# Performance work log

Measured on AMD Instinct MI355X. Metric: run time of the kernel, lower is better.

Reference implementation:

```python
import jax, jax.numpy as jnp
import numpy as np

N = 4096
IN_F = 256
OUT_F = 128
H = 2
ALPHA = 0.2  # leaky relu slope
NEG_INF = -9e15  # matches -9000000000000000.0 in the torch code


def setup_inputs() -> dict:
    key = jax.random.key(0)
    k_x, k_adj, k_w, k_a = jax.random.split(key, 4)
    x = jax.random.normal(k_x, (N, IN_F), dtype=jnp.float32)
    adj = (jax.random.uniform(k_adj, (N, N)) < 0.005).astype(jnp.float32)
    # xavier_uniform with gain=1.414 as in the torch module
    gain = 1.414
    bound_w = gain * np.sqrt(6.0 / (IN_F + OUT_F))
    W = jax.random.uniform(k_w, (H, IN_F, OUT_F), minval=-bound_w, maxval=bound_w, dtype=jnp.float32)
    bound_a = gain * np.sqrt(6.0 / (2 * OUT_F + 1))
    a = jax.random.uniform(k_a, (H, 2 * OUT_F, 1), minval=-bound_a, maxval=bound_a, dtype=jnp.float32)
    return {"x": x, "adj": adj, "W": W, "a": a}


def reference(x, adj, W, a):
    # Dense multi-head GAT layer (eval mode: dropout is identity).
    n = x.shape[0]
    h, _, f_out = W.shape
    adj = adj + jnp.eye(n, dtype=adj.dtype)  # add self loops
    xt = jnp.einsum('nf,hfo->hno', x, W)  # [H, N, F_out]
    # The repeat_interleave/repeat + concat + matmul(a) in the original is
    # exactly the additive decomposition: score[h,i,j] = xt[h,i]@a1[h] + xt[h,j]@a2[h]
    a1 = a[:, :f_out, 0]   # [H, F_out] (applied to target/query node i)
    a2 = a[:, f_out:, 0]   # [H, F_out] (applied to source node j)
    e1 = jnp.einsum('hno,ho->hn', xt, a1)  # [H, N]
    e2 = jnp.einsum('hno,ho->hn', xt, a2)  # [H, N]
    scores = jax.nn.leaky_relu(e1[:, :, None] + e2[:, None, :], negative_slope=ALPHA)  # [H,N,N]
    scores = jnp.where(adj > 0, scores, jnp.asarray(NEG_INF, scores.dtype))
    attn = jax.nn.softmax(scores, axis=-1)
    h_prime = jnp.einsum('hij,hjo->hio', attn, xt)  # [H, N, F_out]
    # concat=True branch: torch .view(N, H*F_out) on contiguous [H,N,F] -> same as reshape
    return jax.nn.elu(h_prime.reshape(n, h * f_out))
```

## Files before the change

kernel.cpp:

```cpp
#include <hip/hip_runtime.h>
#include <math.h>

#define IN_F 256
#define OUT_F 128
#define NHEAD 2
#define ALPHA 0.2f
#define NN 4096
#define NCAP 128

typedef __attribute__((ext_vector_type(8))) short short8;
typedef __attribute__((ext_vector_type(4))) float f32x4;
typedef const __attribute__((address_space(1))) void* gas_ptr;
typedef __attribute__((address_space(3))) void* las_ptr;

__device__ __forceinline__ void async_copy16(const void* g, void* l) {
  __builtin_amdgcn_global_load_lds((gas_ptr)g, (las_ptr)l, 16, 0, 0);
}

__device__ __forceinline__ ushort f2bf(float f) {
  unsigned u = __float_as_uint(f);
  u += 0x7fffu + ((u >> 16) & 1u);
  return (ushort)(u >> 16);
}

__device__ __forceinline__ float lrelu(float t) { return t > 0.f ? t : ALPHA * t; }

__global__ __launch_bounds__(256) void prep_w(
    const float* __restrict__ W, ushort* __restrict__ Wt) {
  int p = blockIdx.x * 256 + threadIdx.x;
  int h = p >> 13;
  int rem = p & 8191;
  int c = rem >> 7;
  int o = rem & 127;
  const float* wsrc = W + h * (IN_F * OUT_F) + (4 * c) * OUT_F + o;
  ushort4 ov;
  ov.x = f2bf(wsrc[0 * OUT_F]);
  ov.y = f2bf(wsrc[1 * OUT_F]);
  ov.z = f2bf(wsrc[2 * OUT_F]);
  ov.w = f2bf(wsrc[3 * OUT_F]);
  *(ushort4*)(Wt + ((size_t)h * OUT_F + o) * IN_F + 4 * c) = ov;
}

__global__ __launch_bounds__(256) void gemm_mfma(
    const float* __restrict__ x, const ushort* __restrict__ Wt,
    const float* __restrict__ a,
    float* __restrict__ xt, float* __restrict__ e1, float* __restrict__ e2) {
  __shared__ ushort sA[32 * 64];
  __shared__ ushort sB[128 * 64];
  __shared__ float sa[2 * OUT_F];
  __shared__ float se1[32], se2[32];

  const int h = blockIdx.y;
  const int rowBase = blockIdx.x * 32;
  const int tid = threadIdx.x;
  const int wave = tid >> 6, lane = tid & 63;
  const int wr = wave & 1, wc = wave >> 1;
  const int q = lane >> 4, l16 = lane & 15;
  const int ar = tid >> 3;
  const int ak = (tid & 7) * 8;

  const float* xrow = x + (size_t)(rowBase + ar) * IN_F + ak;
  float4 ax[8];
#pragma unroll
  for (int c = 0; c < 4; ++c) {
    ax[2 * c]     = *(const float4*)(xrow + 64 * c);
    ax[2 * c + 1] = *(const float4*)(xrow + 64 * c + 4);
  }

  sa[tid] = a[h * (2 * OUT_F) + tid];

  f32x4 acc[4];
#pragma unroll
  for (int i = 0; i < 4; ++i) acc[i] = (f32x4)(0.0f);

  const char* wbase = (const char*)(Wt + (size_t)h * (OUT_F * IN_F));

#pragma unroll
  for (int c = 0; c < 4; ++c) {
    const int k0 = c * 64;
#pragma unroll
    for (int it = 0; it < 4; ++it) {
      int g = it * 256 + tid;
      int r = g >> 3, c8 = g & 7;
      async_copy16(wbase + r * 512 + k0 * 2 + c8 * 16,
                   (char*)sB + (size_t)(it * 256 + wave * 64) * 16);
    }
    {
      float4 va = ax[2 * c], vb = ax[2 * c + 1];
      union { short8 s8; ushort u[8]; } pk;
      pk.u[0] = f2bf(va.x); pk.u[1] = f2bf(va.y);
      pk.u[2] = f2bf(va.z); pk.u[3] = f2bf(va.w);
      pk.u[4] = f2bf(vb.x); pk.u[5] = f2bf(vb.y);
      pk.u[6] = f2bf(vb.z); pk.u[7] = f2bf(vb.w);
      *(short8*)(sA + ar * 64 + ak) = pk.s8;
    }
    __syncthreads();

#pragma unroll
    for (int ks = 0; ks < 64; ks += 32) {
      short8 af = *(const short8*)(sA + (wr * 16 + l16) * 64 + ks + q * 8);
#pragma unroll
      for (int ct = 0; ct < 4; ++ct) {
        int col = wc * 64 + ct * 16 + l16;
        short8 bf = *(const short8*)(sB + col * 64 + ks + q * 8);
        acc[ct] = __builtin_amdgcn_mfma_f32_16x16x32_bf16(af, bf, acc[ct], 0, 0, 0);
      }
    }
    __syncthreads();
  }

#pragma unroll
  for (int ct = 0; ct < 4; ++ct) {
    int col = wc * 64 + ct * 16 + l16;
#pragma unroll
    for (int reg = 0; reg < 4; ++reg) {
      int row = rowBase + wr * 16 + q * 4 + reg;
      xt[((size_t)h * NN + row) * OUT_F + col] = acc[ct][reg];
    }
  }

  float pe1[4], pe2[4];
#pragma unroll
  for (int reg = 0; reg < 4; ++reg) { pe1[reg] = 0.f; pe2[reg] = 0.f; }
#pragma unroll
  for (int ct = 0; ct < 4; ++ct) {
    int col = wc * 64 + ct * 16 + l16;
    float a1v = sa[col], a2v = sa[OUT_F + col];
#pragma unroll
    for (int reg = 0; reg < 4; ++reg) {
      pe1[reg] = fmaf(acc[ct][reg], a1v, pe1[reg]);
      pe2[reg] = fmaf(acc[ct][reg], a2v, pe2[reg]);
    }
  }
#pragma unroll
  for (int off = 1; off < 16; off <<= 1) {
#pragma unroll
    for (int reg = 0; reg < 4; ++reg) {
      pe1[reg] += __shfl_xor(pe1[reg], off, 64);
      pe2[reg] += __shfl_xor(pe2[reg], off, 64);
    }
  }
  if (wc == 0 && l16 == 0) {
#pragma unroll
    for (int reg = 0; reg < 4; ++reg) {
      int r = wr * 16 + q * 4 + reg;
      se1[r] = pe1[reg];
      se2[r] = pe2[reg];
    }
  }
  __syncthreads();
  if (wc == 1 && l16 == 0) {
#pragma unroll
    for (int reg = 0; reg < 4; ++reg) {
      int r = wr * 16 + q * 4 + reg;
      se1[r] += pe1[reg];
      se2[r] += pe2[reg];
    }
  }
  __syncthreads();
  if (tid < 32) {
    e1[(size_t)h * NN + rowBase + tid] = se1[tid];
    e2[(size_t)h * NN + rowBase + tid] = se2[tid];
  }
}

__global__ __launch_bounds__(256) void gat_aggregate(
    const float* __restrict__ adj, const float* __restrict__ xt,
    const float* __restrict__ e1, const float* __restrict__ e2,
    float* __restrict__ out) {
  __shared__ int s_nbr[4][NCAP];
  __shared__ float s_p0[4][NCAP];
  __shared__ float s_p1[4][NCAP];

  const int wave = threadIdx.x >> 6;
  const int lane = threadIdx.x & 63;
  const int i = blockIdx.x * 4 + wave;

  const float4* row4 = (const float4*)(adj + (size_t)i * NN);
  float4 v[16];
#pragma unroll
  for (int c = 0; c < 16; ++c) v[c] = row4[lane + c * 64];

  const unsigned long long lt = (1ull << lane) - 1ull;
  int cnt = 0;
#pragma unroll
  for (int c = 0; c < 16; ++c) {
    float vals[4] = {v[c].x, v[c].y, v[c].z, v[c].w};
#pragma unroll
    for (int s = 0; s < 4; ++s) {
      int j = (c * 64 + lane) * 4 + s;
      bool hit = (vals[s] > 0.f) || (j == i);
      unsigned long long mask = __ballot(hit);
      if (hit) {
        int pos = cnt + (int)__popcll(mask & lt);
        if (pos < NCAP) s_nbr[wave][pos] = j;
      }
      cnt += (int)__popcll(mask);
    }
  }
  const int m = cnt < NCAP ? cnt : NCAP;

  const float e10 = e1[i];
  const float e11 = e1[NN + i];
  float t0[2], t1[2];
  float mx0 = -3.0e38f, mx1 = -3.0e38f;
#pragma unroll
  for (int r = 0; r < 2; ++r) {
    int k = lane + r * 64;
    if (k < m) {
      int j = s_nbr[wave][k];
      t0[r] = lrelu(e10 + e2[j]);
      t1[r] = lrelu(e11 + e2[NN + j]);
      mx0 = fmaxf(mx0, t0[r]);
      mx1 = fmaxf(mx1, t1[r]);
    } else {
      t0[r] = -3.0e38f;
      t1[r] = -3.0e38f;
    }
  }
#pragma unroll
  for (int off = 32; off > 0; off >>= 1) {
    mx0 = fmaxf(mx0, __shfl_xor(mx0, off, 64));
    mx1 = fmaxf(mx1, __shfl_xor(mx1, off, 64));
  }

  float s0 = 0.f, s1 = 0.f;
#pragma unroll
  for (int r = 0; r < 2; ++r) {
    int k = lane + r * 64;
    if (k < m) {
      float p0 = __expf(t0[r] - mx0);
      float p1 = __expf(t1[r] - mx1);
      s_p0[wave][k] = p0;
      s_p1[wave][k] = p1;
      s0 += p0;
      s1 += p1;
    }
  }
#pragma unroll
  for (int off = 32; off > 0; off >>= 1) {
    s0 += __shfl_xor(s0, off, 64);
    s1 += __shfl_xor(s1, off, 64);
  }

  const int h = lane >> 5;
  const int o4 = (lane & 31) * 4;
  const float linv = 1.0f / (h ? s1 : s0);
  const float* pw = h ? s_p1[wave] : s_p0[wave];
  const int* nb = s_nbr[wave];
  const float* xth = xt + (size_t)h * NN * OUT_F + o4;

  f32x4 acc = (f32x4)(0.0f);
  int k = 0;
  for (; k + 4 <= m; k += 4) {
    int j0 = nb[k], j1 = nb[k + 1], j2 = nb[k + 2], j3 = nb[k + 3];
    float w0 = pw[k], w1 = pw[k + 1], w2 = pw[k + 2], w3 = pw[k + 3];
    f32x4 x0 = *(const f32x4*)(xth + (size_t)j0 * OUT_F);
    f32x4 x1 = *(const f32x4*)(xth + (size_t)j1 * OUT_F);
    f32x4 x2 = *(const f32x4*)(xth + (size_t)j2 * OUT_F);
    f32x4 x3 = *(const f32x4*)(xth + (size_t)j3 * OUT_F);
    acc += w0 * x0;
    acc += w1 * x1;
    acc += w2 * x2;
    acc += w3 * x3;
  }
  for (; k < m; ++k) {
    f32x4 xv = *(const f32x4*)(xth + (size_t)nb[k] * OUT_F);
    acc += pw[k] * xv;
  }

  f32x4 r;
#pragma unroll
  for (int e = 0; e < 4; ++e) {
    float av = acc[e] * linv;
    r[e] = av > 0.f ? av : (__expf(av) - 1.0f);
  }
  *(f32x4*)(out + ((size_t)h * NN + i) * OUT_F + o4) = r;
}

extern "C" void kernel_launch(void* const* d_in, const int* in_sizes, int n_in,
                              void* d_out, int out_size, void* d_ws, size_t ws_size,
                              hipStream_t stream) {
  const float* x   = (const float*)d_in[0];
  const float* adj = (const float*)d_in[1];
  const float* W   = (const float*)d_in[2];
  const float* a   = (const float*)d_in[3];
  float* out = (float*)d_out;

  float* xt = (float*)d_ws;
  float* e1 = xt + (size_t)NHEAD * NN * OUT_F;
  float* e2 = e1 + (size_t)NHEAD * NN;
  ushort* Wt = (ushort*)(e2 + (size_t)NHEAD * NN);

  prep_w<<<64, 256, 0, stream>>>(W, Wt);
  gemm_mfma<<<dim3(NN / 32, NHEAD), 256, 0, stream>>>(x, Wt, a, xt, e1, e2);
  gat_aggregate<<<NN / 4, 256, 0, stream>>>(adj, xt, e1, e2, out);
}
```

Baseline: 112.5 us.

## Overlap adjacency scan with projection GEMM and split gather into separate kernel

Moves the adjacency-row neighbour scan out of the aggregation kernel into the GEMM kernel. Every fourth block does a GEMM tile and then scans its rows, while the other blocks only scan. The neighbour lists and counts go to a workspace that a new gather kernel reads. The aim is to hide the 64MB adjacency read behind the GEMM instead of running it serially after it. In exchange it adds extra global writes and reads of the neighbour lists and leaves work unevenly spread across blocks.

Result: slower. 122.0 us (+8.4%).

```diff
diff --git a/kernel.cpp b/kernel.cpp
--- a/kernel.cpp
+++ b/kernel.cpp
@@ -41,140 +41,136 @@
   *(ushort4*)(Wt + ((size_t)h * OUT_F + o) * IN_F + 4 * c) = ov;
 }
 
-__global__ __launch_bounds__(256) void gemm_mfma(
+__global__ __launch_bounds__(256) void gemm_scan(
     const float* __restrict__ x, const ushort* __restrict__ Wt,
-    const float* __restrict__ a,
-    float* __restrict__ xt, float* __restrict__ e1, float* __restrict__ e2) {
+    const float* __restrict__ a, const float* __restrict__ adj,
+    float* __restrict__ xt, float* __restrict__ e1, float* __restrict__ e2,
+    int* __restrict__ nbr, int* __restrict__ cnt) {
   __shared__ ushort sA[32 * 64];
   __shared__ ushort sB[128 * 64];
   __shared__ float sa[2 * OUT_F];
   __shared__ float se1[32], se2[32];
-
-  const int h = blockIdx.y;
-  const int rowBase = blockIdx.x * 32;
+  __shared__ int s_nbr[4][NCAP];
+
+  const int bid = blockIdx.x;
   const int tid = threadIdx.x;
   const int wave = tid >> 6, lane = tid & 63;
-  const int wr = wave & 1, wc = wave >> 1;
-  const int q = lane >> 4, l16 = lane & 15;
-  const int ar = tid >> 3;
-  const int ak = (tid & 7) * 8;
-
-  const float* xrow = x + (size_t)(rowBase + ar) * IN_F + ak;
-  float4 ax[8];
-#pragma unroll
-  for (int c = 0; c < 4; ++c) {
-    ax[2 * c]     = *(const float4*)(xrow + 64 * c);
-    ax[2 * c + 1] = *(const float4*)(xrow + 64 * c + 4);
-  }
-
-  sa[tid] = a[h * (2 * OUT_F) + tid];
-
-  f32x4 acc[4];
-#pragma unroll
-  for (int i = 0; i < 4; ++i) acc[i] = (f32x4)(0.0f);
-
-  const char* wbase = (const char*)(Wt + (size_t)h * (OUT_F * IN_F));
-
-#pragma unroll
-  for (int c = 0; c < 4; ++c) {
-    const int k0 = c * 64;
-#pragma unroll
-    for (int it = 0; it < 4; ++it) {
-      int g = it * 256 + tid;
-      int r = g >> 3, c8 = g & 7;
-      async_copy16(wbase + r * 512 + k0 * 2 + c8 * 16,
-                   (char*)sB + (size_t)(it * 256 + wave * 64) * 16);
-    }
-    {
-      float4 va = ax[2 * c], vb = ax[2 * c + 1];
-      union { short8 s8; ushort u[8]; } pk;
-      pk.u[0] = f2bf(va.x); pk.u[1] = f2bf(va.y);
-      pk.u[2] = f2bf(va.z); pk.u[3] = f2bf(va.w);
-      pk.u[4] = f2bf(vb.x); pk.u[5] = f2bf(vb.y);
-      pk.u[6] = f2bf(vb.z); pk.u[7] = f2bf(vb.w);
-      *(short8*)(sA + ar * 64 + ak) = pk.s8;
+
+  if ((bid & 3) == 0) {
+    const int tile = bid >> 2;
+    const int h = tile >> 7;
+    const int rowBase = (tile & 127) * 32;
+    const int wr = wave & 1, wc = wave >> 1;
+    const int q = lane >> 4, l16 = lane & 15;
+    const int ar = tid >> 3;
+    const int ak = (tid & 7) * 8;
+
+    const float* xrow = x + (size_t)(rowBase + ar) * IN_F + ak;
+    float4 ax[8];
+#pragma unroll
+    for (int c = 0; c < 4; ++c) {
+      ax[2 * c]     = *(const float4*)(xrow + 64 * c);
+      ax[2 * c + 1] = *(const float4*)(xrow + 64 * c + 4);
+    }
+
+    sa[tid] = a[h * (2 * OUT_F) + tid];
+
+    f32x4 acc[4];
+#pragma unroll
+    for (int i = 0; i < 4; ++i) acc[i] = (f32x4)(0.0f);
+
+    const char* wbase = (const char*)(Wt + (size_t)h * (OUT_F * IN_F));
+
+#pragma unroll
+    for (int c = 0; c < 4; ++c) {
+      const int k0 = c * 64;
+#pragma unroll
+      for (int it = 0; it < 4; ++it) {
+        int g = it * 256 + tid;
+        int r = g >> 3, c8 = g & 7;
+        async_copy16(wbase + r * 512 + k0 * 2 + c8 * 16,
+                     (char*)sB + (size_t)(it * 256 + wave * 64) * 16);
+      }
+      {
+        float4 va = ax[2 * c], vb = ax[2 * c + 1];
+        union { short8 s8; ushort u[8]; } pk;
+        pk.u[0] = f2bf(va.x); pk.u[1] = f2bf(va.y);
+        pk.u[2] = f2bf(va.z); pk.u[3] = f2bf(va.w);
+        pk.u[4] = f2bf(vb.x); pk.u[5] = f2bf(vb.y);
+        pk.u[6] = f2bf(vb.z); pk.u[7] = f2bf(vb.w);
+        *(short8*)(sA + ar * 64 + ak) = pk.s8;
+      }
+      __syncthreads();
+
+#pragma unroll
+      for (int ks = 0; ks < 64; ks += 32) {
+        short8 af = *(const short8*)(sA + (wr * 16 + l16) * 64 + ks + q * 8);
+#pragma unroll
+        for (int ct = 0; ct < 4; ++ct) {
+          int col = wc * 64 + ct * 16 + l16;
+          short8 bf = *(const short8*)(sB + col * 64 + ks + q * 8);
+          acc[ct] = __builtin_amdgcn_mfma_f32_16x16x32_bf16(af, bf, acc[ct], 0, 0, 0);
+        }
+      }
+      __syncthreads();
+    }
+
+#pragma unroll
+    for (int ct = 0; ct < 4; ++ct) {
+      int col = wc * 64 + ct * 16 + l16;
+#pragma unroll
+      for (int reg = 0; reg < 4; ++reg) {
+        int row = rowBase + wr * 16 + q * 4 + reg;
+        xt[((size_t)h * NN + row) * OUT_F + col] = acc[ct][reg];
+      }
+    }
+
+    float pe1[4], pe2[4];
+#pragma unroll
+    for (int reg = 0; reg < 4; ++reg) { pe1[reg] = 0.f; pe2[reg] = 0.f; }
+#pragma unroll
+    for (int ct = 0; ct < 4; ++ct) {
+      int col = wc * 64 + ct * 16 + l16;
+      float a1v = sa[col], a2v = sa[OUT_F + col];
+#pragma unroll
+      for (int reg = 0; reg < 4; ++reg) {
+        pe1[reg] = fmaf(acc[ct][reg], a1v, pe1[reg]);
+        pe2[reg] = fmaf(acc[ct][reg], a2v, pe2[reg]);
+      }
+    }
+#pragma unroll
+    for (int off = 1; off < 16; off <<= 1) {
+#pragma unroll
+      for (int reg = 0; reg < 4; ++reg) {
+        pe1[reg] += __shfl_xor(pe1[reg], off, 64);
+        pe2[reg] += __shfl_xor(pe2[reg], off, 64);
+      }
+    }
+    if (wc == 0 && l16 == 0) {
+#pragma unroll
+      for (int reg = 0; reg < 4; ++reg) {
+        int r = wr * 16 + q * 4 + reg;
+        se1[r] = pe1[reg];
+        se2[r] = pe2[reg];
+      }
     }
     __syncthreads();
-
-#pragma unroll
-    for (int ks = 0; ks < 64; ks += 32) {
-      short8 af = *(const short8*)(sA + (wr * 16 + l16) * 64 + ks + q * 8);
-#pragma unroll
-      for (int ct = 0; ct < 4; ++ct) {
-        int col = wc * 64 + ct * 16 + l16;
-        short8 bf = *(const short8*)(sB + col * 64 + ks + q * 8);
-        acc[ct] = __builtin_amdgcn_mfma_f32_16x16x32_bf16(af, bf, acc[ct], 0, 0, 0);
+    if (wc == 1 && l16 == 0) {
+#pragma unroll
+      for (int reg = 0; reg < 4; ++reg) {
+        int r = wr * 16 + q * 4 + reg;
+        se1[r] += pe1[reg];
+        se2[r] += pe2[reg];
       }
     }
     __syncthreads();
-  }
-
-#pragma unroll
-  for (int ct = 0; ct < 4; ++ct) {
-    int col = wc * 64 + ct * 16 + l16;
-#pragma unroll
-    for (int reg = 0; reg < 4; ++reg) {
-      int row = rowBase + wr * 16 + q * 4 + reg;
-      xt[((size_t)h * NN + row) * OUT_F + col] = acc[ct][reg];
-    }
-  }
-
-  float pe1[4], pe2[4];
-#pragma unroll
-  for (int reg = 0; reg < 4; ++reg) { pe1[reg] = 0.f; pe2[reg] = 0.f; }
-#pragma unroll
-  for (int ct = 0; ct < 4; ++ct) {
-    int col = wc * 64 + ct * 16 + l16;
-    float a1v = sa[col], a2v = sa[OUT_F + col];
-#pragma unroll
-    for (int reg = 0; reg < 4; ++reg) {
-      pe1[reg] = fmaf(acc[ct][reg], a1v, pe1[reg]);
-      pe2[reg] = fmaf(acc[ct][reg], a2v, pe2[reg]);
-    }
-  }
-#pragma unroll
-  for (int off = 1; off < 16; off <<= 1) {
-#pragma unroll
-    for (int reg = 0; reg < 4; ++reg) {
-      pe1[reg] += __shfl_xor(pe1[reg], off, 64);
-      pe2[reg] += __shfl_xor(pe2[reg], off, 64);
-    }
-  }
-  if (wc == 0 && l16 == 0) {
-#pragma unroll
-    for (int reg = 0; reg < 4; ++reg) {
-      int r = wr * 16 + q * 4 + reg;
-      se1[r] = pe1[reg];
-      se2[r] = pe2[reg];
-    }
-  }
-  __syncthreads();
-  if (wc == 1 && l16 == 0) {
-#pragma unroll
-    for (int reg = 0; reg < 4; ++reg) {
-      int r = wr * 16 + q * 4 + reg;
-      se1[r] += pe1[reg];
-      se2[r] += pe2[reg];
-    }
-  }
-  __syncthreads();
-  if (tid < 32) {
-    e1[(size_t)h * NN + rowBase + tid] = se1[tid];
-    e2[(size_t)h * NN + rowBase + tid] = se2[tid];
-  }
-}
-
-__global__ __launch_bounds__(256) void gat_aggregate(
-    const float* __restrict__ adj, const float* __restrict__ xt,
-    const float* __restrict__ e1, const float* __restrict__ e2,
-    float* __restrict__ out) {
-  __shared__ int s_nbr[4][NCAP];
-  __shared__ float s_p0[4][NCAP];
-  __shared__ float s_p1[4][NCAP];
-
-  const int wave = threadIdx.x >> 6;
-  const int lane = threadIdx.x & 63;
-  const int i = blockIdx.x * 4 + wave;
+    if (tid < 32) {
+      e1[(size_t)h * NN + rowBase + tid] = se1[tid];
+      e2[(size_t)h * NN + rowBase + tid] = se2[tid];
+    }
+  }
+
+  const int i = bid * 4 + wave;
 
   const float4* row4 = (const float4*)(adj + (size_t)i * NN);
   float4 v[16];
@@ -182,7 +178,7 @@
   for (int c = 0; c < 16; ++c) v[c] = row4[lane + c * 64];
 
   const unsigned long long lt = (1ull << lane) - 1ull;
-  int cnt = 0;
+  int total = 0;
 #pragma unroll
   for (int c = 0; c < 16; ++c) {
     float vals[4] = {v[c].x, v[c].y, v[c].z, v[c].w};
@@ -192,13 +188,45 @@
       bool hit = (vals[s] > 0.f) || (j == i);
       unsigned long long mask = __ballot(hit);
       if (hit) {
-        int pos = cnt + (int)__popcll(mask & lt);
+        int pos = total + (int)__popcll(mask & lt);
         if (pos < NCAP) s_nbr[wave][pos] = j;
       }
-      cnt += (int)__popcll(mask);
-    }
-  }
-  const int m = cnt < NCAP ? cnt : NCAP;
+      total += (int)__popcll(mask);
+    }
+  }
+  const int m = total < NCAP ? total : NCAP;
+#pragma unroll
+  for (int r = 0; r < 2; ++r) {
+    int k = lane + r * 64;
+    if (k < m) nbr[(size_t)i * NCAP + k] = s_nbr[wave][k];
+  }
+  if (lane == 0) cnt[i] = m;
+}
+
+__global__ __launch_bounds__(256) void gat_gather(
+    const float* __restrict__ xt, const float* __restrict__ e1,
+    const float* __restrict__ e2, const int* __restrict__ nbr,
+    const int* __restrict__ cnt, float* __restrict__ out) {
+  __shared__ int s_nbr[4][NCAP];
+  __shared__ float s_p0[4][NCAP];
+  __shared__ float s_p1[4][NCAP];
+
+  const int wave = threadIdx.x >> 6;
+  const int lane = threadIdx.x & 63;
+  const int i = blockIdx.x * 4 + wave;
+
+  const int m = cnt[i];
+
+  int jr[2] = {0, 0};
+#pragma unroll
+  for (int r = 0; r < 2; ++r) {
+    int k = lane + r * 64;
+    if (k < m) {
+      int j = nbr[(size_t)i * NCAP + k];
+      jr[r] = j;
+      s_nbr[wave][k] = j;
+    }
+  }
 
   const float e10 = e1[i];
   const float e11 = e1[NN + i];
@@ -208,7 +236,7 @@
   for (int r = 0; r < 2; ++r) {
     int k = lane + r * 64;
     if (k < m) {
-      int j = s_nbr[wave][k];
+      int j = jr[r];
       t0[r] = lrelu(e10 + e2[j]);
       t1[r] = lrelu(e11 + e2[NN + j]);
       mx0 = fmaxf(mx0, t0[r]);
@@ -291,8 +319,10 @@
   float* e1 = xt + (size_t)NHEAD * NN * OUT_F;
   float* e2 = e1 + (size_t)NHEAD * NN;
   ushort* Wt = (ushort*)(e2 + (size_t)NHEAD * NN);
+  int* nbr = (int*)(Wt + (size_t)NHEAD * OUT_F * IN_F);
+  int* cnt = nbr + (size_t)NN * NCAP;
 
   prep_w<<<64, 256, 0, stream>>>(W, Wt);
-  gemm_mfma<<<dim3(NN / 32, NHEAD), 256, 0, stream>>>(x, Wt, a, xt, e1, e2);
-  gat_aggregate<<<NN / 4, 256, 0, stream>>>(adj, xt, e1, e2, out);
-}
+  gemm_scan<<<1024, 256, 0, stream>>>(x, Wt, a, adj, xt, e1, e2, nbr, cnt);
+  gat_gather<<<NN / 4, 256, 0, stream>>>(xt, e1, e2, nbr, cnt, out);
+}
```
